# Kernel optimization log

Measured on AMD Instinct MI355X. Metric: run time of the kernel, lower is better.

## Reference

```python
import jax, jax.numpy as jnp
import numpy as np

N_VOX = 200000
C_IN = 64
C_OUT = 128
GRID = (480, 360, 32)  # (D, H, W) cylindrical voxel grid
LRELU_SLOPE = 0.01
BN_EPS = 1e-5

OFFSETS_31 = [(dz, 0, dx) for dz in (-1, 0, 1) for dx in (-1, 0, 1)]  # kernel (3,1,3)
OFFSETS_13 = [(0, dy, dx) for dy in (-1, 0, 1) for dx in (-1, 0, 1)]  # kernel (1,3,3)


def _build_neighbors(coords, offsets, grid):
    """coords: [N,3] int. Returns [K,N] int32 neighbor indices, N = sentinel (inactive)."""
    D, H, W = grid
    n = coords.shape[0]
    lookup = np.full(D * H * W, -1, dtype=np.int64)
    lin = (coords[:, 0] * H + coords[:, 1]) * W + coords[:, 2]
    lookup[lin] = np.arange(n)
    nbrs = []
    for off in offsets:
        c = coords + np.asarray(off)
        valid = (c[:, 0] >= 0) & (c[:, 0] < D) & (c[:, 1] >= 0) & (c[:, 1] < H) & (c[:, 2] >= 0) & (c[:, 2] < W)
        l = np.clip((c[:, 0] * H + c[:, 1]) * W + c[:, 2], 0, D * H * W - 1)
        idx = np.where(valid, lookup[l], -1)
        nbrs.append(np.where(idx < 0, n, idx))
    return np.stack(nbrs).astype(np.int32)


def setup_inputs() -> dict:
    key = jax.random.key(0)
    ks = jax.random.split(key, 8)
    rng = np.random.default_rng(0)
    D, H, W = GRID
    lin = rng.choice(D * H * W, size=N_VOX, replace=False)
    coords = np.stack([lin // (H * W), (lin // W) % H, lin % W], axis=1)
    nbr31 = jnp.asarray(_build_neighbors(coords, OFFSETS_31, GRID))
    nbr13 = jnp.asarray(_build_neighbors(coords, OFFSETS_13, GRID))

    def kaiming(k, kk, cin, cout):
        return jax.random.normal(k, (kk, cin, cout), jnp.float32) * np.float32(1.0 / np.sqrt(kk * cin))

    return {
        "features": jax.random.normal(ks[0], (N_VOX, C_IN), jnp.float32),
        "nbr31": nbr31,
        "nbr13": nbr13,
        "W_conv1": kaiming(ks[1], 9, C_IN, C_OUT),
        "W_conv1_2": kaiming(ks[2], 9, C_OUT, C_OUT),
        "W_conv2": kaiming(ks[3], 9, C_IN, C_OUT),
        "W_conv3": kaiming(ks[4], 9, C_OUT, C_OUT),
        "g0": jnp.ones((C_OUT,), jnp.float32), "b0": jnp.zeros((C_OUT,), jnp.float32),
        "g0_2": jnp.ones((C_OUT,), jnp.float32), "b0_2": jnp.zeros((C_OUT,), jnp.float32),
        "g1": jnp.ones((C_OUT,), jnp.float32), "b1": jnp.zeros((C_OUT,), jnp.float32),
        "g2": jnp.ones((C_OUT,), jnp.float32), "b2": jnp.zeros((C_OUT,), jnp.float32),
    }


def _submconv(f, nbr, W):
    """Submanifold sparse conv: f [N,Cin], nbr [K,N] (N=sentinel), W [K,Cin,Cout]."""
    f_pad = jnp.concatenate([f, jnp.zeros((1, f.shape[1]), f.dtype)], axis=0)
    out = jnp.zeros((f.shape[0], W.shape[2]), f.dtype)
    for k in range(W.shape[0]):  # fixed K=9 kernel taps
        out = out + f_pad[nbr[k]] @ W[k]
    return out


def _lrelu(x):
    return jnp.where(x >= 0, x, LRELU_SLOPE * x)


def _bn(x, g, b):
    # BatchNorm1d, training mode: batch stats over active voxels (biased var)
    m = jnp.mean(x, axis=0)
    v = jnp.var(x, axis=0)
    return (x - m) * jax.lax.rsqrt(v + BN_EPS) * g + b


def reference(features, nbr31, nbr13, W_conv1, W_conv1_2, W_conv2, W_conv3,
              g0, b0, g0_2, b0_2, g1, b1, g2, b2):
    # shortcut branch: conv3x1 -> lrelu -> bn -> conv1x3 -> lrelu -> bn
    s = _submconv(features, nbr31, W_conv1)
    s = _bn(_lrelu(s), g0, b0)
    s = _submconv(s, nbr13, W_conv1_2)
    s = _bn(_lrelu(s), g0_2, b0_2)
    # main branch: conv1x3 -> lrelu -> bn -> conv3x1 -> lrelu -> bn
    r = _submconv(features, nbr13, W_conv2)
    r = _bn(_lrelu(r), g1, b1)
    r = _submconv(r, nbr31, W_conv3)
    r = _bn(_lrelu(r), g2, b2)
    return r + s
```

## Files before the change

### kernel.cpp

```cpp
#include <hip/hip_runtime.h>
#include <hip/hip_bf16.h>

typedef unsigned short u16;
typedef unsigned int u32;
typedef __attribute__((ext_vector_type(8))) short s16x8;
typedef __attribute__((ext_vector_type(4))) short s16x4;
typedef __attribute__((ext_vector_type(4))) float f32x4;

__device__ inline u16 f2bf(float x) {
    u32 u = __float_as_uint(x);
    u32 r = (u + 0x7fffu + ((u >> 16) & 1u)) >> 16;
    return (u16)r;
}
__device__ inline float bf2f(u16 u) {
    return __uint_as_float(((u32)u) << 16);
}

__global__ void k_feat2bf(const float* __restrict__ f, u16* __restrict__ o,
                          int total, int nvalid) {
    int i = (blockIdx.x * 256 + threadIdx.x) * 8;
    if (i >= total) return;
    s16x8 v;
#pragma unroll
    for (int j = 0; j < 8; ++j) {
        float x = (i + j < nvalid) ? f[i + j] : 0.f;
        v[j] = (short)f2bf(x);
    }
    *(s16x8*)(o + i) = v;
}

__global__ void k_swz(const float* __restrict__ W, u16* __restrict__ o, int cin) {
    int i = blockIdx.x * 256 + threadIdx.x;
    int total = 9 * cin * 128;
    if (i >= total) return;
    int j = i & 7;
    int l = (i >> 3) & 63;
    int fr = i >> 9;
    int ct = fr & 7;
    int rest = fr >> 3;
    int kcn = cin >> 5;
    int kc = rest % kcn;
    int t = rest / kcn;
    int kk = kc * 32 + (l >> 4) * 8 + j;
    int c = ct * 16 + (l & 15);
    o[i] = f2bf(W[(t * cin + kk) * 128 + c]);
}

template <int CIN>
__global__ __launch_bounds__(1024, 4) void k_conv(
    const u16* __restrict__ srcA, const u16* __restrict__ srcB,
    const int* __restrict__ nbrA, const int* __restrict__ nbrB,
    const u16* __restrict__ wA, const u16* __restrict__ wB,
    u16* __restrict__ zoutA, u16* __restrict__ zoutB,
    float* __restrict__ statsA, float* __restrict__ statsB,
    int N) {
    constexpr int KC = CIN / 32;
    constexpr int FR = 9 * KC * 2;
    __shared__ u16 wl[FR * 512];
    __shared__ float sstat[64];

    const int nvr = (N + 511) >> 9;
    const int npairs = 2 * nvr;
    const int i = blockIdx.x;
    const int c8 = i & 7;
    const int m = i >> 3;
    const int h = m & 3;
    const int q = m >> 2;
    const int p = 8 * q + c8;
    if (p >= npairs) return;
    const int vr = p % nvr;
    const int cz = p / nvr;
    const int half = h;

    const u16* __restrict__ src = cz ? srcB : srcA;
    const int* __restrict__ nbr = cz ? nbrB : nbrA;
    const u16* __restrict__ w = cz ? wB : wA;
    u16* __restrict__ zout = cz ? zoutB : zoutA;
    float* __restrict__ stats = cz ? statsB : statsA;

    const int tid = threadIdx.x;

    for (int ii = tid; ii < FR * 64; ii += 1024) {
        int pp = ii & 63;
        int f = ii >> 6;
        int ctp = f & 1;
        int tk = f >> 1;
        s16x8 v = *(const s16x8*)(w + ((size_t)(tk * 8 + half * 2 + ctp)) * 512 + pp * 8);
        *(s16x8*)&wl[(size_t)f * 512 + pp * 8] = v;
    }
    if (tid < 64) sstat[tid] = 0.f;
    __syncthreads();

    const int lane = tid & 63;
    const int wv = tid >> 6;
    const int base = vr * 512 + wv * 32;
    const int am = lane & 15;
    const int grp = lane >> 4;
    const int vi0 = base + am;
    const int vi1 = base + 16 + am;

    int r0[9], r1[9];
#pragma unroll
    for (int t = 0; t < 9; ++t) {
        r0[t] = (vi0 < N) ? nbr[t * N + vi0] : N;
        r1[t] = (vi1 < N) ? nbr[t * N + vi1] : N;
    }

    f32x4 acc0[2], acc1[2];
#pragma unroll
    for (int c = 0; c < 2; ++c) {
        acc0[c] = (f32x4){0.f, 0.f, 0.f, 0.f};
        acc1[c] = (f32x4){0.f, 0.f, 0.f, 0.f};
    }

#pragma unroll
    for (int t = 0; t < 9; ++t) {
        if (__any((r0[t] != N) || (r1[t] != N))) {
            const u16* sp0 = src + (size_t)r0[t] * CIN + grp * 8;
            const u16* sp1 = src + (size_t)r1[t] * CIN + grp * 8;
            s16x8 a0[KC], a1[KC];
#pragma unroll
            for (int kc = 0; kc < KC; ++kc) {
                a0[kc] = *(const s16x8*)(sp0 + kc * 32);
                a1[kc] = *(const s16x8*)(sp1 + kc * 32);
            }
            const u16* lb = wl + (size_t)t * (KC * 2) * 512 + lane * 8;
#pragma unroll
            for (int kc = 0; kc < KC; ++kc) {
#pragma unroll
                for (int c = 0; c < 2; ++c) {
                    s16x8 b = *(const s16x8*)(lb + (kc * 2 + c) * 512);
                    acc0[c] = __builtin_amdgcn_mfma_f32_16x16x32_bf16(a0[kc], b, acc0[c], 0, 0, 0);
                    acc1[c] = __builtin_amdgcn_mfma_f32_16x16x32_bf16(a1[kc], b, acc1[c], 0, 0, 0);
                }
            }
        }
    }

#pragma unroll
    for (int c = 0; c < 2; ++c) {
        float s = 0.f, qq = 0.f;
        const int col = half * 32 + c * 16 + am;
#pragma unroll
        for (int j = 0; j < 4; ++j) {
            {
                float x = acc0[c][j];
                float z = (x > 0.f) ? x : 0.01f * x;
                int row = base + grp * 4 + j;
                if (row < N) zout[(size_t)row * 128 + col] = f2bf(z);
                s += z;
                qq += z * z;
            }
            {
                float x = acc1[c][j];
                float z = (x > 0.f) ? x : 0.01f * x;
                int row = base + 16 + grp * 4 + j;
                if (row < N) zout[(size_t)row * 128 + col] = f2bf(z);
                s += z;
                qq += z * z;
            }
        }
        s += __shfl_xor(s, 16);
        qq += __shfl_xor(qq, 16);
        s += __shfl_xor(s, 32);
        qq += __shfl_xor(qq, 32);
        if (lane < 16) {
            atomicAdd(&sstat[c * 16 + am], s);
            atomicAdd(&sstat[32 + c * 16 + am], qq);
        }
    }
    __syncthreads();
    if (tid < 32) {
        int cg = half * 32 + tid;
        atomicAdd(stats + cg, sstat[tid]);
        atomicAdd(stats + 128 + cg, sstat[32 + tid]);
    }
}

__global__ void k_fin(const float* __restrict__ stats,
                      const float* __restrict__ g0, const float* __restrict__ b0,
                      const float* __restrict__ g1, const float* __restrict__ b1,
                      float* __restrict__ ss, int N) {
    int tid = threadIdx.x;
    int set = tid >> 7, c = tid & 127;
    const float* st = stats + set * 256;
    float invN = 1.f / (float)N;
    float m = st[c] * invN;
    float var = st[128 + c] * invN - m * m;
    const float* g = set ? g1 : g0;
    const float* b = set ? b1 : b0;
    float sc = g[c] * rsqrtf(var + 1e-5f);
    float sh = b[c] - m * sc;
    float* o = ss + set * 256;
    o[c] = sc;
    o[128 + c] = sh;
}

__global__ void k_aff(const u16* __restrict__ z, const float* __restrict__ ss,
                      u16* __restrict__ y, int N) {
    int v = blockIdx.x * 256 + threadIdx.x;
    int total = (N + 1) * 16;
    if (v >= total) return;
    int row = v >> 4;
    int cb = (v & 15) * 8;
    s16x8 o;
    if (row < N) {
        s16x8 zi = *(const s16x8*)(z + (size_t)row * 128 + cb);
#pragma unroll
        for (int j = 0; j < 8; ++j) {
            float x = bf2f((u16)zi[j]);
            float r = x * ss[cb + j] + ss[128 + cb + j];
            o[j] = (short)f2bf(r);
        }
    } else {
        o = (s16x8){0, 0, 0, 0, 0, 0, 0, 0};
    }
    *(s16x8*)(y + (size_t)row * 128 + cb) = o;
}

__global__ void k_final(const u16* __restrict__ z3, const u16* __restrict__ z4,
                        const float* __restrict__ ssA, const float* __restrict__ ssB,
                        float* __restrict__ out, int N) {
    int v = blockIdx.x * 256 + threadIdx.x;
    int total = N * 32;
    if (v >= total) return;
    int row = v >> 5;
    int cb = (v & 31) * 4;
    s16x4 a = *(const s16x4*)(z3 + (size_t)row * 128 + cb);
    s16x4 b = *(const s16x4*)(z4 + (size_t)row * 128 + cb);
    f32x4 o;
#pragma unroll
    for (int j = 0; j < 4; ++j) {
        int c = cb + j;
        o[j] = bf2f((u16)a[j]) * ssA[c] + ssA[128 + c] +
               bf2f((u16)b[j]) * ssB[c] + ssB[128 + c];
    }
    *(f32x4*)(out + (size_t)row * 128 + cb) = o;
}

extern "C" void kernel_launch(void* const* d_in, const int* in_sizes, int n_in,
                              void* d_out, int out_size, void* d_ws, size_t ws_size,
                              hipStream_t stream) {
    const float* feat = (const float*)d_in[0];
    const int* nbr31 = (const int*)d_in[1];
    const int* nbr13 = (const int*)d_in[2];
    const float* W1 = (const float*)d_in[3];
    const float* W12 = (const float*)d_in[4];
    const float* W2 = (const float*)d_in[5];
    const float* W3 = (const float*)d_in[6];
    const float* g0 = (const float*)d_in[7];
    const float* b0 = (const float*)d_in[8];
    const float* g02 = (const float*)d_in[9];
    const float* b02 = (const float*)d_in[10];
    const float* g1 = (const float*)d_in[11];
    const float* b1 = (const float*)d_in[12];
    const float* g2 = (const float*)d_in[13];
    const float* b2 = (const float*)d_in[14];
    float* out = (float*)d_out;
    const int N = in_sizes[0] / 64;

    char* p = (char*)d_ws;
    auto alloc = [&](size_t bytes) {
        char* r = p;
        p += (bytes + 255) & ~(size_t)255;
        return r;
    };
    float* stats = (float*)alloc(4 * 256 * sizeof(float));
    float* ss = (float*)alloc(4 * 256 * sizeof(float));
    u16* featbf = (u16*)alloc((size_t)(N + 1) * 64 * 2);
    u16* w1 = (u16*)alloc((size_t)9 * 64 * 128 * 2);
    u16* w2 = (u16*)alloc((size_t)9 * 64 * 128 * 2);
    u16* w12 = (u16*)alloc((size_t)9 * 128 * 128 * 2);
    u16* w3 = (u16*)alloc((size_t)9 * 128 * 128 * 2);
    u16* zA = (u16*)alloc((size_t)N * 128 * 2);
    u16* zB = (u16*)alloc((size_t)N * 128 * 2);
    u16* y1 = (u16*)alloc((size_t)(N + 1) * 128 * 2);
    u16* y2 = (u16*)alloc((size_t)(N + 1) * 128 * 2);

    hipMemsetAsync(stats, 0, 4 * 256 * sizeof(float), stream);

    int totF = (N + 1) * 64;
    k_feat2bf<<<(totF / 8 + 255) / 256, 256, 0, stream>>>(feat, featbf, totF, N * 64);
    k_swz<<<(9 * 64 * 128 + 255) / 256, 256, 0, stream>>>(W1, w1, 64);
    k_swz<<<(9 * 64 * 128 + 255) / 256, 256, 0, stream>>>(W2, w2, 64);
    k_swz<<<(9 * 128 * 128 + 255) / 256, 256, 0, stream>>>(W12, w12, 128);
    k_swz<<<(9 * 128 * 128 + 255) / 256, 256, 0, stream>>>(W3, w3, 128);

    int nvr = (N + 511) / 512;
    int npairs = 2 * nvr;
    int nblk = 8 * 4 * ((npairs + 7) / 8);

    k_conv<64><<<nblk, 1024, 0, stream>>>(
        featbf, featbf, nbr31, nbr13, w1, w2, zA, zB, stats + 0, stats + 256, N);
    k_fin<<<1, 256, 0, stream>>>(stats, g0, b0, g1, b1, ss, N);
    int ablk = ((N + 1) * 16 + 255) / 256;
    k_aff<<<ablk, 256, 0, stream>>>(zA, ss + 0, y1, N);
    k_aff<<<ablk, 256, 0, stream>>>(zB, ss + 256, y2, N);
    k_conv<128><<<nblk, 1024, 0, stream>>>(
        y1, y2, nbr13, nbr31, w12, w3, zA, zB, stats + 512, stats + 768, N);
    k_fin<<<1, 256, 0, stream>>>(stats + 512, g02, b02, g2, b2, ss + 512, N);
    k_final<<<(N * 32 + 255) / 256, 256, 0, stream>>>(zA, zB, ss + 512, ss + 768, out, N);
}
```

Before: 407.0 us.

## Widen conv blocks to 64 output columns and double-buffer neighbor gathers

Each block now computes 64 output channels instead of 32, halving the block count and the number of times each gathered input row is re-read across column splits. The gather loop is software-pipelined: the next tap's feature rows are loaded while the current tap's MFMAs run, and neighbor indices are fetched two taps ahead and broadcast via shuffles instead of being loaded all up front. MFMAs are also skipped per 16-row half when that half has no active neighbors. This raises register and LDS use, and the 4-waves/SIMD occupancy hint is dropped, which may lower occupancy.

```diff
diff --git a/kernel.cpp b/kernel.cpp
--- a/kernel.cpp
+++ b/kernel.cpp
@@ -3,6 +3,7 @@
 
 typedef unsigned short u16;
 typedef unsigned int u32;
+typedef unsigned long long u64;
 typedef __attribute__((ext_vector_type(8))) short s16x8;
 typedef __attribute__((ext_vector_type(4))) short s16x4;
 typedef __attribute__((ext_vector_type(4))) float f32x4;
@@ -47,7 +48,7 @@
 }
 
 template <int CIN>
-__global__ __launch_bounds__(1024, 4) void k_conv(
+__global__ __launch_bounds__(1024) void k_conv(
     const u16* __restrict__ srcA, const u16* __restrict__ srcB,
     const int* __restrict__ nbrA, const int* __restrict__ nbrB,
     const u16* __restrict__ wA, const u16* __restrict__ wB,
@@ -55,22 +56,22 @@
     float* __restrict__ statsA, float* __restrict__ statsB,
     int N) {
     constexpr int KC = CIN / 32;
-    constexpr int FR = 9 * KC * 2;
+    constexpr int FR = 9 * KC * 4;
     __shared__ u16 wl[FR * 512];
-    __shared__ float sstat[64];
+    __shared__ float sstat[128];
 
     const int nvr = (N + 511) >> 9;
     const int npairs = 2 * nvr;
     const int i = blockIdx.x;
     const int c8 = i & 7;
     const int m = i >> 3;
-    const int h = m & 3;
-    const int q = m >> 2;
+    const int h = m & 1;
+    const int q = m >> 1;
     const int p = 8 * q + c8;
     if (p >= npairs) return;
     const int vr = p % nvr;
     const int cz = p / nvr;
-    const int half = h;
+    const int colset = h;
 
     const u16* __restrict__ src = cz ? srcB : srcA;
     const int* __restrict__ nbr = cz ? nbrB : nbrA;
@@ -83,12 +84,12 @@
     for (int ii = tid; ii < FR * 64; ii += 1024) {
         int pp = ii & 63;
         int f = ii >> 6;
-        int ctp = f & 1;
-        int tk = f >> 1;
-        s16x8 v = *(const s16x8*)(w + ((size_t)(tk * 8 + half * 2 + ctp)) * 512 + pp * 8);
+        int c = f & 3;
+        int tk = f >> 2;
+        s16x8 v = *(const s16x8*)(w + ((size_t)(tk * 8 + colset * 4 + c)) * 512 + pp * 8);
         *(s16x8*)&wl[(size_t)f * 512 + pp * 8] = v;
     }
-    if (tid < 64) sstat[tid] = 0.f;
+    if (tid < 128) sstat[tid] = 0.f;
     __syncthreads();
 
     const int lane = tid & 63;
@@ -96,51 +97,73 @@
     const int base = vr * 512 + wv * 32;
     const int am = lane & 15;
     const int grp = lane >> 4;
-    const int vi0 = base + am;
-    const int vi1 = base + 16 + am;
-
-    int r0[9], r1[9];
-#pragma unroll
-    for (int t = 0; t < 9; ++t) {
-        r0[t] = (vi0 < N) ? nbr[t * N + vi0] : N;
-        r1[t] = (vi1 < N) ? nbr[t * N + vi1] : N;
-    }
-
-    f32x4 acc0[2], acc1[2];
-#pragma unroll
-    for (int c = 0; c < 2; ++c) {
+    const int vi = base + (lane & 31);
+    const bool vok = vi < N;
+
+    int rc = vok ? nbr[vi] : N;
+    int rn = vok ? nbr[N + vi] : N;
+
+    s16x8 a[2][2][KC];
+    {
+        int rg0 = __shfl(rc, am);
+        int rg1 = __shfl(rc, 16 + am);
+        const u16* sp0 = src + (size_t)rg0 * CIN + grp * 8;
+        const u16* sp1 = src + (size_t)rg1 * CIN + grp * 8;
+#pragma unroll
+        for (int kc = 0; kc < KC; ++kc) {
+            a[0][0][kc] = *(const s16x8*)(sp0 + kc * 32);
+            a[0][1][kc] = *(const s16x8*)(sp1 + kc * 32);
+        }
+    }
+
+    f32x4 acc0[4], acc1[4];
+#pragma unroll
+    for (int c = 0; c < 4; ++c) {
         acc0[c] = (f32x4){0.f, 0.f, 0.f, 0.f};
         acc1[c] = (f32x4){0.f, 0.f, 0.f, 0.f};
     }
 
 #pragma unroll
     for (int t = 0; t < 9; ++t) {
-        if (__any((r0[t] != N) || (r1[t] != N))) {
-            const u16* sp0 = src + (size_t)r0[t] * CIN + grp * 8;
-            const u16* sp1 = src + (size_t)r1[t] * CIN + grp * 8;
-            s16x8 a0[KC], a1[KC];
+        const int cur = t & 1, nxt = cur ^ 1;
+        if (t < 8) {
+            int rg0 = __shfl(rn, am);
+            int rg1 = __shfl(rn, 16 + am);
+            const u16* sp0 = src + (size_t)rg0 * CIN + grp * 8;
+            const u16* sp1 = src + (size_t)rg1 * CIN + grp * 8;
 #pragma unroll
             for (int kc = 0; kc < KC; ++kc) {
-                a0[kc] = *(const s16x8*)(sp0 + kc * 32);
-                a1[kc] = *(const s16x8*)(sp1 + kc * 32);
+                a[nxt][0][kc] = *(const s16x8*)(sp0 + kc * 32);
+                a[nxt][1][kc] = *(const s16x8*)(sp1 + kc * 32);
             }
-            const u16* lb = wl + (size_t)t * (KC * 2) * 512 + lane * 8;
+        }
+        int rf = N;
+        if (t < 7 && vok) rf = nbr[(t + 2) * N + vi];
+        __builtin_amdgcn_sched_barrier(0);
+
+        u64 mask = __ballot(rc != N);
+        if (mask != 0ULL) {
+            const bool e0 = (mask & 0xFFFFull) != 0;
+            const bool e1 = (mask & 0xFFFF0000ull) != 0;
+            const u16* lb = wl + (size_t)t * (KC * 4) * 512 + lane * 8;
 #pragma unroll
             for (int kc = 0; kc < KC; ++kc) {
 #pragma unroll
-                for (int c = 0; c < 2; ++c) {
-                    s16x8 b = *(const s16x8*)(lb + (kc * 2 + c) * 512);
-                    acc0[c] = __builtin_amdgcn_mfma_f32_16x16x32_bf16(a0[kc], b, acc0[c], 0, 0, 0);
-                    acc1[c] = __builtin_amdgcn_mfma_f32_16x16x32_bf16(a1[kc], b, acc1[c], 0, 0, 0);
+                for (int c = 0; c < 4; ++c) {
+                    s16x8 b = *(const s16x8*)(lb + (size_t)(kc * 4 + c) * 512);
+                    if (e0) acc0[c] = __builtin_amdgcn_mfma_f32_16x16x32_bf16(a[cur][0][kc], b, acc0[c], 0, 0, 0);
+                    if (e1) acc1[c] = __builtin_amdgcn_mfma_f32_16x16x32_bf16(a[cur][1][kc], b, acc1[c], 0, 0, 0);
                 }
             }
         }
-    }
-
-#pragma unroll
-    for (int c = 0; c < 2; ++c) {
+        rc = rn;
+        rn = rf;
+    }
+
+#pragma unroll
+    for (int c = 0; c < 4; ++c) {
         float s = 0.f, qq = 0.f;
-        const int col = half * 32 + c * 16 + am;
+        const int col = colset * 64 + c * 16 + am;
 #pragma unroll
         for (int j = 0; j < 4; ++j) {
             {
@@ -166,14 +189,14 @@
         qq += __shfl_xor(qq, 32);
         if (lane < 16) {
             atomicAdd(&sstat[c * 16 + am], s);
-            atomicAdd(&sstat[32 + c * 16 + am], qq);
+            atomicAdd(&sstat[64 + c * 16 + am], qq);
         }
     }
     __syncthreads();
-    if (tid < 32) {
-        int cg = half * 32 + tid;
+    if (tid < 64) {
+        int cg = colset * 64 + tid;
         atomicAdd(stats + cg, sstat[tid]);
-        atomicAdd(stats + 128 + cg, sstat[32 + tid]);
+        atomicAdd(stats + 128 + cg, sstat[64 + tid]);
     }
 }
 
@@ -288,7 +311,7 @@
 
     int nvr = (N + 511) / 512;
     int npairs = 2 * nvr;
-    int nblk = 8 * 4 * ((npairs + 7) / 8);
+    int nblk = 8 * 2 * ((npairs + 7) / 8);
 
     k_conv<64><<<nblk, 1024, 0, stream>>>(
         featbf, featbf, nbr31, nbr13, w1, w2, zA, zB, stats + 0, stats + 256, N);
```

After: 1.559 ms. 3.83x slower.
